# Optimization experiments

Hardware: AMD Instinct MI355X
Metric: run time of the kernel (lower is better)

The kernel has to match this reference:

```python
import jax, jax.numpy as jnp
import numpy as np

B, T, IN, H, OUT = 128, 512, 64, 1024, 1


def _glorot(key, shape, fan_in):
    # mimic nn.Linear default init scale (uniform +-1/sqrt(fan_in))
    bound = 1.0 / np.sqrt(fan_in)
    return jax.random.uniform(key, shape, jnp.float32, -bound, bound)


def setup_inputs() -> dict:
    key = jax.random.key(0)
    ks = jax.random.split(key, 20)
    inp = {
        "x": jax.random.normal(ks[0], (B, T, IN), jnp.float32),
        "boundary": jax.random.normal(ks[1], (B, 2), jnp.float32),
        # layer 0: stacked gate weights, order [i, f, o, g]
        "Wx0": _glorot(ks[2], (4 * H, IN), IN),
        "bx0": _glorot(ks[3], (4 * H,), IN),
        "Uh0": _glorot(ks[4], (4 * H, H), H),
        "bh0": _glorot(ks[5], (4 * H,), H),
        "Wb0": _glorot(ks[6], (H, 2), 2),
        "bb0": _glorot(ks[7], (H,), 2),
        # layer 1
        "Wx1": _glorot(ks[8], (4 * H, H), H),
        "bx1": _glorot(ks[9], (4 * H,), H),
        "Uh1": _glorot(ks[10], (4 * H, H), H),
        "bh1": _glorot(ks[11], (4 * H,), H),
        "Wb1": _glorot(ks[12], (H, 2), 2),
        "bb1": _glorot(ks[13], (H, 2)[:1], 2),
        # output head
        "fcW": _glorot(ks[14], (OUT, H), H),
        "fcb": _glorot(ks[15], (OUT,), H),
    }
    return inp


def _cell(gates, f_extra, c_prev):
    # gates: [B, 4H] pre-activations in order i,f,o,g
    i, f, o, g = jnp.split(gates, 4, axis=-1)
    i = jax.nn.sigmoid(i)
    f = jax.nn.sigmoid(f + f_extra)
    o = jax.nn.sigmoid(o)
    g = jnp.tanh(g)
    c = f * c_prev + i * g
    h = o * jnp.tanh(c)
    return h, c


def reference(x, boundary, Wx0, bx0, Uh0, bh0, Wb0, bb0,
              Wx1, bx1, Uh1, bh1, Wb1, bb1, fcW, fcb):
    batch = x.shape[0]
    Hdim = fcW.shape[1]
    # precompute input projections for layer 0 over all timesteps: [T,B,4H]
    xp0 = jnp.einsum('bti,gi->tbg', x, Wx0) + bx0
    # boundary influence on forget gate, constant over time: [B,H]
    bi0 = boundary @ Wb0.T + bb0
    bi1 = boundary @ Wb1.T + bb1

    zeros = jnp.zeros((batch, Hdim), x.dtype)
    carry0 = (zeros, zeros, zeros, zeros)  # h0, c0, h1, c1

    def step(carry, xp_t):
        h0, c0, h1, c1 = carry
        g0 = xp_t + h0 @ Uh0.T + bh0
        h0n, c0n = _cell(g0, bi0, c0)
        g1 = h0n @ Wx1.T + bx1 + h1 @ Uh1.T + bh1
        h1n, c1n = _cell(g1, bi1, c1)
        return (h0n, c0n, h1n, c1n), None

    (h0, c0, h1, c1), _ = jax.lax.scan(step, carry0, xp0)
    # fc applied to last timestep's top-layer hidden state
    return h1 @ fcW.T + fcb
```

## Files before the change

kernel.cpp:

```cpp
#include <hip/hip_runtime.h>
#include <math.h>


#define Hd 1024
#define Bd 128
#define Td 512
#define INd 64
#define NWG 256
#define NTHR 512

typedef _Float16 f16;
typedef _Float16 half8 __attribute__((ext_vector_type(8)));
typedef float f32x4 __attribute__((ext_vector_type(4)));


__device__ __forceinline__ float fsigm(float x) {
    return __fdividef(1.f, 1.f + __expf(-x));
}
__device__ __forceinline__ float ftanh_(float x) {
    return 1.f - __fdividef(2.f, 1.f + __expf(2.f * x));
}

__global__ __launch_bounds__(512) void init_state(
    const float* __restrict__ bnd, const float* __restrict__ Wb0,
    const float* __restrict__ bb0, const float* __restrict__ Wb1,
    const float* __restrict__ bb1,
    float* __restrict__ bi0, float* __restrict__ bi1,
    f16* __restrict__ h0buf, f16* __restrict__ h1buf,
    unsigned int* __restrict__ sync)
{
    int idx = blockIdx.x * 512 + threadIdx.x;
    int b = idx >> 10;
    int h = idx & 1023;
    float b0v = bnd[b * 2 + 0], b1v = bnd[b * 2 + 1];
    bi0[idx] = b0v * Wb0[h * 2 + 0] + b1v * Wb0[h * 2 + 1] + bb0[h];
    bi1[idx] = b0v * Wb1[h * 2 + 0] + b1v * Wb1[h * 2 + 1] + bb1[h];
    h0buf[idx] = (f16)0.f;  h0buf[idx + Bd * Hd] = (f16)0.f;
    h1buf[idx] = (f16)0.f;  h1buf[idx + Bd * Hd] = (f16)0.f;
    if (idx < 640) sync[idx] = 0u;
}

__global__ __launch_bounds__(512) void xpose(
    const float* __restrict__ x, f16* __restrict__ xT)
{
    int idx = blockIdx.x * 512 + threadIdx.x;
    int b = idx >> 15;
    int t = (idx >> 6) & 511;
    int i = idx & 63;
    xT[((size_t)t * Bd + b) * INd + i] = (f16)x[idx];
}

__global__ __launch_bounds__(NTHR, 2) void lstm_persist(
    const f16* __restrict__ xT,
    f16* __restrict__ h0buf, f16* __restrict__ h1buf,
    const float* __restrict__ bi0, const float* __restrict__ bi1,
    const float* __restrict__ Wx0, const float* __restrict__ bx0,
    const float* __restrict__ Uh0, const float* __restrict__ bh0,
    const float* __restrict__ Wx1, const float* __restrict__ bx1,
    const float* __restrict__ Uh1, const float* __restrict__ bh1,
    const float* __restrict__ fcW, const float* __restrict__ fcb,
    float* __restrict__ out, unsigned int* __restrict__ sync)
{
    const int tid  = threadIdx.x;
    const int w    = tid >> 6;
    const int lane = tid & 63;
    const int n    = lane & 15;
    const int q    = lane >> 4;
    const int wg   = blockIdx.x;
    const int c0wg = wg * 4;
    const int hcol = c0wg + (n & 3);
    const int gid  = n >> 2;
    const bool lowhalf = (w < 4);
    const int p    = lowhalf ? w : (w - 4);
    const int mt   = lowhalf ? 2 * p : 2 * p + 1;
    const size_t S = (size_t)Bd * Hd;

    __shared__ f16 B0[16 * 1096];
    __shared__ float xchg[3072];

    const bool glead = ((wg & 31) == 0);
    unsigned int* garr = sync + 32 + 32 * (wg >> 5);
    int  xcd  = 0;
    bool lead = false;
    unsigned int* relp = nullptr;
    if (tid == 0) {
        asm volatile("s_getreg_b32 %0, hwreg(HW_REG_XCC_ID)" : "=s"(xcd));
        xcd &= 7;
        unsigned r = __hip_atomic_fetch_add(&sync[608 + xcd], 1u,
                         __ATOMIC_RELAXED, __HIP_MEMORY_SCOPE_AGENT);
        lead = (r == 0u);
        relp = sync + 288 + 32 * xcd;
    }

    {
        int nr = tid >> 5;
        int gr = (nr >> 2) * Hd + c0wg + (nr & 3);
        for (int k = tid & 31; k < 1088; k += 32) {
            float v = (k < Hd) ? Uh0[(size_t)gr * Hd + k]
                               : Wx0[(size_t)gr * INd + (k - Hd)];
            B0[nr * 1096 + k] = (f16)v;
        }
    }

    half8 b1f[32];
    {
        const float* Wsrc = lowhalf ? Wx1 : Uh1;
        int gr = gid * Hd + c0wg + (n & 3);
        const float* rp = Wsrc + (size_t)gr * Hd + q * 8;
        #pragma unroll
        for (int kk = 0; kk < 32; ++kk) {
            half8 hv;
            #pragma unroll
            for (int j = 0; j < 8; ++j) hv[j] = (f16)rp[kk * 32 + j];
            b1f[kk] = hv;
        }
    }

    float gb0[4], gb1[4], bia0[4], bia1[4];
    #pragma unroll
    for (int g = 0; g < 4; ++g) {
        gb0[g] = bx0[g * Hd + hcol] + bh0[g * Hd + hcol];
        gb1[g] = bx1[g * Hd + hcol] + bh1[g * Hd + hcol];
    }
    #pragma unroll
    for (int r = 0; r < 4; ++r) {
        int row = mt * 16 + q * 4 + r;
        bia0[r] = bi0[row * Hd + hcol];
        bia1[r] = bi1[row * Hd + hcol];
    }
    f32x4 c0v = {0.f, 0.f, 0.f, 0.f};
    f32x4 c1v = {0.f, 0.f, 0.f, 0.f};

    __syncthreads();

    unsigned epoch = 0;

    for (int s = -1; s <= 511; ++s) {
        const bool do_l0 = (s < 511);
        const bool do_l1 = (s >= 0);
        const int pr = s & 1;
        const f16* h0r = h0buf + (size_t)pr * S;
        f16*       h0w = h0buf + (size_t)(1 - pr) * S;
        const f16* h1r = h1buf + (size_t)(1 - pr) * S;
        f16*       h1w = h1buf + (size_t)pr * S;

        f32x4 a0a = {0.f,0.f,0.f,0.f}, a0b = {0.f,0.f,0.f,0.f};
        f32x4 a1a = {0.f,0.f,0.f,0.f}, a1b = {0.f,0.f,0.f,0.f};

        if (lowhalf) {
            const half8* pA0 = (const half8*)(h0r + (size_t)(2*p*16 + n) * Hd + q*8);
            const half8* pA1 = (const half8*)(h0r + (size_t)((2*p+1)*16 + n) * Hd + q*8);
            const half8* pB  = (const half8*)(&B0[n * 1096 + q * 8]);
            if (do_l0 && do_l1) {
                #pragma unroll
                for (int kk = 0; kk < 32; ++kk) {
                    half8 A0 = pA0[kk*4], A1 = pA1[kk*4], Bl = pB[kk*4];
                    a0a = __builtin_amdgcn_mfma_f32_16x16x32_f16(A0, Bl, a0a, 0,0,0);
                    a0b = __builtin_amdgcn_mfma_f32_16x16x32_f16(A1, Bl, a0b, 0,0,0);
                    a1a = __builtin_amdgcn_mfma_f32_16x16x32_f16(A0, b1f[kk], a1a, 0,0,0);
                    a1b = __builtin_amdgcn_mfma_f32_16x16x32_f16(A1, b1f[kk], a1b, 0,0,0);
                }
            } else if (do_l0) {
                #pragma unroll
                for (int kk = 0; kk < 32; ++kk) {
                    half8 A0 = pA0[kk*4], A1 = pA1[kk*4], Bl = pB[kk*4];
                    a0a = __builtin_amdgcn_mfma_f32_16x16x32_f16(A0, Bl, a0a, 0,0,0);
                    a0b = __builtin_amdgcn_mfma_f32_16x16x32_f16(A1, Bl, a0b, 0,0,0);
                }
            } else {
                #pragma unroll
                for (int kk = 0; kk < 32; ++kk) {
                    half8 A0 = pA0[kk*4], A1 = pA1[kk*4];
                    a1a = __builtin_amdgcn_mfma_f32_16x16x32_f16(A0, b1f[kk], a1a, 0,0,0);
                    a1b = __builtin_amdgcn_mfma_f32_16x16x32_f16(A1, b1f[kk], a1b, 0,0,0);
                }
            }
            if (do_l0) {
                const f16* xt = xT + (size_t)(s + 1) * Bd * INd;
                const half8* pX0 = (const half8*)(xt + (size_t)(2*p*16 + n) * INd + q*8);
                const half8* pX1 = (const half8*)(xt + (size_t)((2*p+1)*16 + n) * INd + q*8);
                #pragma unroll
                for (int kk = 0; kk < 2; ++kk) {
                    half8 Bl = pB[(32 + kk) * 4];
                    a0a = __builtin_amdgcn_mfma_f32_16x16x32_f16(pX0[kk*4], Bl, a0a, 0,0,0);
                    a0b = __builtin_amdgcn_mfma_f32_16x16x32_f16(pX1[kk*4], Bl, a0b, 0,0,0);
                }
            }
        } else if (do_l1) {
            const half8* pH1a = (const half8*)(h1r + (size_t)(2*p*16 + n) * Hd + q*8);
            const half8* pH1b = (const half8*)(h1r + (size_t)((2*p+1)*16 + n) * Hd + q*8);
            #pragma unroll
            for (int kk = 0; kk < 32; ++kk) {
                half8 A0 = pH1a[kk*4], A1 = pH1b[kk*4];
                a1a = __builtin_amdgcn_mfma_f32_16x16x32_f16(A0, b1f[kk], a1a, 0,0,0);
                a1b = __builtin_amdgcn_mfma_f32_16x16x32_f16(A1, b1f[kk], a1b, 0,0,0);
            }
        }

        float* slotA = xchg;
        float* slotB = xchg + 1024;
        float* slotC = xchg + 2048;
        if (lowhalf) {
            if (do_l0) *(f32x4*)&slotA[p * 256 + lane * 4] = a0b;
            if (do_l1) *(f32x4*)&slotB[p * 256 + lane * 4] = a1b;
        } else {
            if (do_l1) *(f32x4*)&slotC[p * 256 + lane * 4] = a1a;
        }
        __syncthreads();

        f32x4 g0acc, g1acc;
        if (lowhalf) {
            g0acc = a0a;
            if (do_l1) g1acc = a1a + *(const f32x4*)&slotC[p * 256 + lane * 4];
        } else {
            if (do_l0) g0acc = *(const f32x4*)&slotA[p * 256 + lane * 4];
            if (do_l1) g1acc = a1b + *(const f32x4*)&slotB[p * 256 + lane * 4];
        }

        auto cell = [&](f32x4 acc, const float* gb, const float* bia,
                        f32x4& cst, f16* hw) {
            #pragma unroll
            for (int r = 0; r < 4; ++r) {
                float own = acc[r];
                float v4  = __shfl_xor(own, 4);
                float v8  = __shfl_xor(own, 8);
                float v12 = __shfl_xor(own, 12);
                float ip = gid==0?own: gid==1?v4 : gid==2?v8 : v12;
                float fp = gid==0?v4 : gid==1?own: gid==2?v12: v8;
                float op = gid==0?v8 : gid==1?v12: gid==2?own: v4;
                float gp = gid==0?v12: gid==1?v8 : gid==2?v4 : own;
                float I = fsigm(ip + gb[0]);
                float F = fsigm(fp + gb[1] + bia[r]);
                float O = fsigm(op + gb[2]);
                float G = ftanh_(gp + gb[3]);
                float c = F * cst[r] + I * G;
                cst[r] = c;
                float h = O * ftanh_(c);
                if (n < 4) {
                    union { f16 hf; unsigned short us; } cv; cv.hf = (f16)h;
                    __hip_atomic_store(
                        (unsigned short*)&hw[(size_t)(mt * 16 + q * 4 + r) * Hd + c0wg + n],
                        cv.us, __ATOMIC_RELAXED, __HIP_MEMORY_SCOPE_AGENT);
                }
            }
        };
        if (do_l0) cell(g0acc, gb0, bia0, c0v, h0w);
        if (do_l1) cell(g1acc, gb1, bia1, c1v, h1w);

        __syncthreads();
        if (tid == 0) {
            const unsigned tgt = epoch + 1u;
            __hip_atomic_fetch_add(garr, 1u, __ATOMIC_RELAXED,
                                   __HIP_MEMORY_SCOPE_AGENT);
            if (glead) {
                while (__hip_atomic_load(garr, __ATOMIC_RELAXED,
                                         __HIP_MEMORY_SCOPE_AGENT) < 32u * tgt)
                    __builtin_amdgcn_s_sleep(1);
                __hip_atomic_fetch_add(sync, 32u, __ATOMIC_RELAXED,
                                       __HIP_MEMORY_SCOPE_AGENT);
            }
            if (lead) {
                while (__hip_atomic_load(sync, __ATOMIC_RELAXED,
                                         __HIP_MEMORY_SCOPE_AGENT) < NWG * tgt)
                    __builtin_amdgcn_s_sleep(1);
                asm volatile("buffer_inv sc1\n\ts_waitcnt vmcnt(0)" ::: "memory");
                __hip_atomic_store(relp, tgt, __ATOMIC_RELAXED,
                                   __HIP_MEMORY_SCOPE_AGENT);
            } else {
                while (__hip_atomic_load(relp, __ATOMIC_RELAXED,
                                         __HIP_MEMORY_SCOPE_AGENT) < tgt)
                    __builtin_amdgcn_s_sleep(1);
                asm volatile("buffer_inv\n\ts_waitcnt vmcnt(0)" ::: "memory");
            }
        }
        epoch++;
        __syncthreads();
    }

    if (blockIdx.x < Bd) {
        int b = blockIdx.x;
        const f16* hf = h1buf + S + (size_t)b * Hd;
        int k = tid * 2;
        float sum = (float)hf[k] * fcW[k] + (float)hf[k + 1] * fcW[k + 1];
        #pragma unroll
        for (int off = 32; off > 0; off >>= 1) sum += __shfl_down(sum, off);
        float* red = xchg;
        if (lane == 0) red[w] = sum;
        __syncthreads();
        if (tid == 0) {
            float t = 0.f;
            #pragma unroll
            for (int i = 0; i < 8; ++i) t += red[i];
            out[b] = t + fcb[0];
        }
    }
}

extern "C" void kernel_launch(void* const* d_in, const int* in_sizes, int n_in,
                              void* d_out, int out_size, void* d_ws, size_t ws_size,
                              hipStream_t stream) {
    const float* x        = (const float*)d_in[0];
    const float* boundary = (const float*)d_in[1];
    const float* Wx0      = (const float*)d_in[2];
    const float* bx0      = (const float*)d_in[3];
    const float* Uh0      = (const float*)d_in[4];
    const float* bh0      = (const float*)d_in[5];
    const float* Wb0      = (const float*)d_in[6];
    const float* bb0      = (const float*)d_in[7];
    const float* Wx1      = (const float*)d_in[8];
    const float* bx1      = (const float*)d_in[9];
    const float* Uh1      = (const float*)d_in[10];
    const float* bh1      = (const float*)d_in[11];
    const float* Wb1      = (const float*)d_in[12];
    const float* bb1      = (const float*)d_in[13];
    const float* fcW      = (const float*)d_in[14];
    const float* fcb      = (const float*)d_in[15];
    float* out = (float*)d_out;

    char* ws = (char*)d_ws;
    f16*   xT    = (f16*)(ws);
    f16*   h0buf = (f16*)(ws + 8388608);
    f16*   h1buf = (f16*)(ws + 8912896);
    float* bi0   = (float*)(ws + 9437184);
    float* bi1   = (float*)(ws + 9961472);
    unsigned int* sync = (unsigned int*)(ws + 10485760);

    init_state<<<256, 512, 0, stream>>>(boundary, Wb0, bb0, Wb1, bb1,
                                        bi0, bi1, h0buf, h1buf, sync);
    xpose<<<8192, 512, 0, stream>>>(x, xT);

    void* args[] = {
        (void*)&xT, (void*)&h0buf, (void*)&h1buf, (void*)&bi0, (void*)&bi1,
        (void*)&Wx0, (void*)&bx0, (void*)&Uh0, (void*)&bh0,
        (void*)&Wx1, (void*)&bx1, (void*)&Uh1, (void*)&bh1,
        (void*)&fcW, (void*)&fcb, (void*)&out, (void*)&sync
    };
    hipLaunchCooperativeKernel((void*)lstm_persist, dim3(NWG), dim3(NTHR),
                               args, 0, stream);
}
```

Baseline: 11.00 ms.

## Retile persistent LSTM to 8 hidden columns by 64 batch rows per workgroup

Workgroups now split work as pairs: each covers 8 hidden columns (all four gates, laid out as two 16-wide N tiles) and half the batch, rather than 4 columns across the full batch. Each wave loads one A fragment per k step and reuses it across two B tiles. Layer 0 is handled entirely by the low waves and layer 1 by the high waves, which cuts the LDS exchange to a single layer-1 partial sum and replaces the three-way gate shuffle with one xor-8 shuffle. The cost is twice the LDS for layer-0 weights and two register-resident layer-1 weight fragments per lane, which raises register pressure under the 2-waves launch bound and may cause spills.

```diff
diff --git a/kernel.cpp b/kernel.cpp
--- a/kernel.cpp
+++ b/kernel.cpp
@@ -67,16 +67,17 @@
     const int n    = lane & 15;
     const int q    = lane >> 4;
     const int wg   = blockIdx.x;
-    const int c0wg = wg * 4;
-    const int hcol = c0wg + (n & 3);
-    const int gid  = n >> 2;
+    const int gb   = wg >> 1;
+    const int bh   = wg & 1;
+    const int hc0  = gb * 8;
+    const int hcol = hc0 + (n & 7);
     const bool lowhalf = (w < 4);
     const int p    = lowhalf ? w : (w - 4);
-    const int mt   = lowhalf ? 2 * p : 2 * p + 1;
+    const int bt   = bh * 64 + p * 16;
     const size_t S = (size_t)Bd * Hd;
 
-    __shared__ f16 B0[16 * 1096];
-    __shared__ float xchg[3072];
+    __shared__ f16 B0[32 * 1096];
+    __shared__ float xchg[2048];
 
     const bool glead = ((wg & 31) == 0);
     unsigned int* garr = sync + 32 + 32 * (wg >> 5);
@@ -93,26 +94,33 @@
     }
 
     {
-        int nr = tid >> 5;
-        int gr = (nr >> 2) * Hd + c0wg + (nr & 3);
-        for (int k = tid & 31; k < 1088; k += 32) {
+        int nr = tid >> 4;
+        int t  = nr >> 4, np = nr & 15;
+        int gr = (t * 2 + (np >> 3)) * Hd + hc0 + (np & 7);
+        for (int k = tid & 15; k < 1088; k += 16) {
             float v = (k < Hd) ? Uh0[(size_t)gr * Hd + k]
                                : Wx0[(size_t)gr * INd + (k - Hd)];
             B0[nr * 1096 + k] = (f16)v;
         }
     }
 
-    half8 b1f[32];
+    half8 b1f0[32], b1f1[32];
     {
         const float* Wsrc = lowhalf ? Wx1 : Uh1;
-        int gr = gid * Hd + c0wg + (n & 3);
-        const float* rp = Wsrc + (size_t)gr * Hd + q * 8;
+        int gr0 = (0 + (n >> 3)) * Hd + hcol;
+        int gr1 = (2 + (n >> 3)) * Hd + hcol;
+        const float* rp0 = Wsrc + (size_t)gr0 * Hd + q * 8;
+        const float* rp1 = Wsrc + (size_t)gr1 * Hd + q * 8;
         #pragma unroll
         for (int kk = 0; kk < 32; ++kk) {
-            half8 hv;
+            half8 h0v, h1v;
             #pragma unroll
-            for (int j = 0; j < 8; ++j) hv[j] = (f16)rp[kk * 32 + j];
-            b1f[kk] = hv;
+            for (int j = 0; j < 8; ++j) {
+                h0v[j] = (f16)rp0[kk * 32 + j];
+                h1v[j] = (f16)rp1[kk * 32 + j];
+            }
+            b1f0[kk] = h0v;
+            b1f1[kk] = h1v;
         }
     }
 
@@ -124,9 +132,9 @@
     }
     #pragma unroll
     for (int r = 0; r < 4; ++r) {
-        int row = mt * 16 + q * 4 + r;
-        bia0[r] = bi0[row * Hd + hcol];
-        bia1[r] = bi1[row * Hd + hcol];
+        int row = bt + q * 4 + r;
+        bia0[r] = bi0[(size_t)row * Hd + hcol];
+        bia1[r] = bi1[(size_t)row * Hd + hcol];
     }
     f32x4 c0v = {0.f, 0.f, 0.f, 0.f};
     f32x4 c1v = {0.f, 0.f, 0.f, 0.f};
@@ -148,104 +156,89 @@
         f32x4 a1a = {0.f,0.f,0.f,0.f}, a1b = {0.f,0.f,0.f,0.f};
 
         if (lowhalf) {
-            const half8* pA0 = (const half8*)(h0r + (size_t)(2*p*16 + n) * Hd + q*8);
-            const half8* pA1 = (const half8*)(h0r + (size_t)((2*p+1)*16 + n) * Hd + q*8);
-            const half8* pB  = (const half8*)(&B0[n * 1096 + q * 8]);
+            const half8* pA  = (const half8*)(h0r + (size_t)(bt + n) * Hd + q*8);
+            const half8* pB0t = (const half8*)(&B0[n        * 1096 + q * 8]);
+            const half8* pB1t = (const half8*)(&B0[(16 + n) * 1096 + q * 8]);
             if (do_l0 && do_l1) {
                 #pragma unroll
                 for (int kk = 0; kk < 32; ++kk) {
-                    half8 A0 = pA0[kk*4], A1 = pA1[kk*4], Bl = pB[kk*4];
-                    a0a = __builtin_amdgcn_mfma_f32_16x16x32_f16(A0, Bl, a0a, 0,0,0);
-                    a0b = __builtin_amdgcn_mfma_f32_16x16x32_f16(A1, Bl, a0b, 0,0,0);
-                    a1a = __builtin_amdgcn_mfma_f32_16x16x32_f16(A0, b1f[kk], a1a, 0,0,0);
-                    a1b = __builtin_amdgcn_mfma_f32_16x16x32_f16(A1, b1f[kk], a1b, 0,0,0);
+                    half8 A = pA[kk*4];
+                    a0a = __builtin_amdgcn_mfma_f32_16x16x32_f16(A, pB0t[kk*4], a0a, 0,0,0);
+                    a0b = __builtin_amdgcn_mfma_f32_16x16x32_f16(A, pB1t[kk*4], a0b, 0,0,0);
+                    a1a = __builtin_amdgcn_mfma_f32_16x16x32_f16(A, b1f0[kk], a1a, 0,0,0);
+                    a1b = __builtin_amdgcn_mfma_f32_16x16x32_f16(A, b1f1[kk], a1b, 0,0,0);
                 }
             } else if (do_l0) {
                 #pragma unroll
                 for (int kk = 0; kk < 32; ++kk) {
-                    half8 A0 = pA0[kk*4], A1 = pA1[kk*4], Bl = pB[kk*4];
-                    a0a = __builtin_amdgcn_mfma_f32_16x16x32_f16(A0, Bl, a0a, 0,0,0);
-                    a0b = __builtin_amdgcn_mfma_f32_16x16x32_f16(A1, Bl, a0b, 0,0,0);
+                    half8 A = pA[kk*4];
+                    a0a = __builtin_amdgcn_mfma_f32_16x16x32_f16(A, pB0t[kk*4], a0a, 0,0,0);
+                    a0b = __builtin_amdgcn_mfma_f32_16x16x32_f16(A, pB1t[kk*4], a0b, 0,0,0);
                 }
             } else {
                 #pragma unroll
                 for (int kk = 0; kk < 32; ++kk) {
-                    half8 A0 = pA0[kk*4], A1 = pA1[kk*4];
-                    a1a = __builtin_amdgcn_mfma_f32_16x16x32_f16(A0, b1f[kk], a1a, 0,0,0);
-                    a1b = __builtin_amdgcn_mfma_f32_16x16x32_f16(A1, b1f[kk], a1b, 0,0,0);
+                    half8 A = pA[kk*4];
+                    a1a = __builtin_amdgcn_mfma_f32_16x16x32_f16(A, b1f0[kk], a1a, 0,0,0);
+                    a1b = __builtin_amdgcn_mfma_f32_16x16x32_f16(A, b1f1[kk], a1b, 0,0,0);
                 }
             }
             if (do_l0) {
                 const f16* xt = xT + (size_t)(s + 1) * Bd * INd;
-                const half8* pX0 = (const half8*)(xt + (size_t)(2*p*16 + n) * INd + q*8);
-                const half8* pX1 = (const half8*)(xt + (size_t)((2*p+1)*16 + n) * INd + q*8);
+                const half8* pX = (const half8*)(xt + (size_t)(bt + n) * INd + q*8);
                 #pragma unroll
                 for (int kk = 0; kk < 2; ++kk) {
-                    half8 Bl = pB[(32 + kk) * 4];
-                    a0a = __builtin_amdgcn_mfma_f32_16x16x32_f16(pX0[kk*4], Bl, a0a, 0,0,0);
-                    a0b = __builtin_amdgcn_mfma_f32_16x16x32_f16(pX1[kk*4], Bl, a0b, 0,0,0);
+                    half8 X = pX[kk*4];
+                    a0a = __builtin_amdgcn_mfma_f32_16x16x32_f16(X, pB0t[(32+kk)*4], a0a, 0,0,0);
+                    a0b = __builtin_amdgcn_mfma_f32_16x16x32_f16(X, pB1t[(32+kk)*4], a0b, 0,0,0);
                 }
             }
         } else if (do_l1) {
-            const half8* pH1a = (const half8*)(h1r + (size_t)(2*p*16 + n) * Hd + q*8);
-            const half8* pH1b = (const half8*)(h1r + (size_t)((2*p+1)*16 + n) * Hd + q*8);
+            const half8* pH = (const half8*)(h1r + (size_t)(bt + n) * Hd + q*8);
             #pragma unroll
             for (int kk = 0; kk < 32; ++kk) {
-                half8 A0 = pH1a[kk*4], A1 = pH1b[kk*4];
-                a1a = __builtin_amdgcn_mfma_f32_16x16x32_f16(A0, b1f[kk], a1a, 0,0,0);
-                a1b = __builtin_amdgcn_mfma_f32_16x16x32_f16(A1, b1f[kk], a1b, 0,0,0);
-            }
-        }
-
-        float* slotA = xchg;
-        float* slotB = xchg + 1024;
-        float* slotC = xchg + 2048;
-        if (lowhalf) {
-            if (do_l0) *(f32x4*)&slotA[p * 256 + lane * 4] = a0b;
-            if (do_l1) *(f32x4*)&slotB[p * 256 + lane * 4] = a1b;
-        } else {
-            if (do_l1) *(f32x4*)&slotC[p * 256 + lane * 4] = a1a;
+                half8 A = pH[kk*4];
+                a1a = __builtin_amdgcn_mfma_f32_16x16x32_f16(A, b1f0[kk], a1a, 0,0,0);
+                a1b = __builtin_amdgcn_mfma_f32_16x16x32_f16(A, b1f1[kk], a1b, 0,0,0);
+            }
+        }
+
+        if (lowhalf && do_l1) {
+            *(f32x4*)&xchg[p * 512 +       lane * 4] = a1a;
+            *(f32x4*)&xchg[p * 512 + 256 + lane * 4] = a1b;
         }
         __syncthreads();
-
-        f32x4 g0acc, g1acc;
-        if (lowhalf) {
-            g0acc = a0a;
-            if (do_l1) g1acc = a1a + *(const f32x4*)&slotC[p * 256 + lane * 4];
-        } else {
-            if (do_l0) g0acc = *(const f32x4*)&slotA[p * 256 + lane * 4];
-            if (do_l1) g1acc = a1b + *(const f32x4*)&slotB[p * 256 + lane * 4];
-        }
-
-        auto cell = [&](f32x4 acc, const float* gb, const float* bia,
-                        f32x4& cst, f16* hw) {
+        f32x4 g1a, g1b;
+        if (!lowhalf && do_l1) {
+            g1a = a1a + *(const f32x4*)&xchg[p * 512 +       lane * 4];
+            g1b = a1b + *(const f32x4*)&xchg[p * 512 + 256 + lane * 4];
+        }
+
+        auto cell = [&](f32x4 accA, f32x4 accB, const float* gbx,
+                        const float* bia, f32x4& cst, f16* hw) {
             #pragma unroll
             for (int r = 0; r < 4; ++r) {
-                float own = acc[r];
-                float v4  = __shfl_xor(own, 4);
-                float v8  = __shfl_xor(own, 8);
-                float v12 = __shfl_xor(own, 12);
-                float ip = gid==0?own: gid==1?v4 : gid==2?v8 : v12;
-                float fp = gid==0?v4 : gid==1?own: gid==2?v12: v8;
-                float op = gid==0?v8 : gid==1?v12: gid==2?own: v4;
-                float gp = gid==0?v12: gid==1?v8 : gid==2?v4 : own;
-                float I = fsigm(ip + gb[0]);
-                float F = fsigm(fp + gb[1] + bia[r]);
-                float O = fsigm(op + gb[2]);
-                float G = ftanh_(gp + gb[3]);
+                float t0  = accA[r];
+                float t1  = accB[r];
+                float t0x = __shfl_xor(t0, 8);
+                float t1x = __shfl_xor(t1, 8);
+                float I = fsigm(t0  + gbx[0]);
+                float F = fsigm(t0x + gbx[1] + bia[r]);
+                float O = fsigm(t1  + gbx[2]);
+                float G = ftanh_(t1x + gbx[3]);
                 float c = F * cst[r] + I * G;
                 cst[r] = c;
                 float h = O * ftanh_(c);
-                if (n < 4) {
+                if (n < 8) {
                     union { f16 hf; unsigned short us; } cv; cv.hf = (f16)h;
                     __hip_atomic_store(
-                        (unsigned short*)&hw[(size_t)(mt * 16 + q * 4 + r) * Hd + c0wg + n],
+                        (unsigned short*)&hw[(size_t)(bt + q * 4 + r) * Hd + hc0 + n],
                         cv.us, __ATOMIC_RELAXED, __HIP_MEMORY_SCOPE_AGENT);
                 }
             }
         };
-        if (do_l0) cell(g0acc, gb0, bia0, c0v, h0w);
-        if (do_l1) cell(g1acc, gb1, bia1, c1v, h1w);
+        if (lowhalf) { if (do_l0) cell(a0a, a0b, gb0, bia0, c0v, h0w); }
+        else         { if (do_l1) cell(g1a, g1b, gb1, bia1, c1v, h1w); }
 
         __syncthreads();
         if (tid == 0) {
```

New measurement: 10.75 ms. 1.02x faster.

## Double workgroup to 16 waves, each wave owns one row tile, weights in LDS

Applied to the files above, without the earlier changes.

Workgroups grow from 8 to 16 waves. Each wave now handles a single 16-row batch tile instead of two, so the per-step MFMA chain per wave is roughly halved. The Wx1/Uh1 weight fragments move from per-wave registers into a larger shared buffer (48 rows), along with Uh0/Wx0. Layer-0 and layer-1 cells are split across the two wave halves, and only the layer-1 partial sums are exchanged through LDS. The costs are more LDS traffic (weights are reread every step), a roughly 105 KB LDS footprint, and a launch-bounds hint of 4 that is optimistic for 1024-thread blocks.

```diff
diff --git a/kernel.cpp b/kernel.cpp
--- a/kernel.cpp
+++ b/kernel.cpp
@@ -7,7 +7,7 @@
 #define Td 512
 #define INd 64
 #define NWG 256
-#define NTHR 512
+#define NTHR 1024
 
 typedef _Float16 f16;
 typedef _Float16 half8 __attribute__((ext_vector_type(8)));
@@ -50,7 +50,7 @@
     xT[((size_t)t * Bd + b) * INd + i] = (f16)x[idx];
 }
 
-__global__ __launch_bounds__(NTHR, 2) void lstm_persist(
+__global__ __launch_bounds__(NTHR, 4) void lstm_persist(
     const f16* __restrict__ xT,
     f16* __restrict__ h0buf, f16* __restrict__ h1buf,
     const float* __restrict__ bi0, const float* __restrict__ bi1,
@@ -70,13 +70,12 @@
     const int c0wg = wg * 4;
     const int hcol = c0wg + (n & 3);
     const int gid  = n >> 2;
-    const bool lowhalf = (w < 4);
-    const int p    = lowhalf ? w : (w - 4);
-    const int mt   = lowhalf ? 2 * p : 2 * p + 1;
+    const bool lowhalf = (w < 8);
+    const int p    = lowhalf ? w : (w - 8);
     const size_t S = (size_t)Bd * Hd;
 
-    __shared__ f16 B0[16 * 1096];
-    __shared__ float xchg[3072];
+    __shared__ f16 WL[48 * 1096];
+    __shared__ float xchg[2048];
 
     const bool glead = ((wg & 31) == 0);
     unsigned int* garr = sync + 32 + 32 * (wg >> 5);
@@ -93,43 +92,37 @@
     }
 
     {
-        int nr = tid >> 5;
-        int gr = (nr >> 2) * Hd + c0wg + (nr & 3);
-        for (int k = tid & 31; k < 1088; k += 32) {
-            float v = (k < Hd) ? Uh0[(size_t)gr * Hd + k]
-                               : Wx0[(size_t)gr * INd + (k - Hd)];
-            B0[nr * 1096 + k] = (f16)v;
-        }
-    }
-
-    half8 b1f[32];
+        int nr = tid >> 4;
+        if (nr < 48) {
+            int loc = nr & 15;
+            int gr = (loc >> 2) * Hd + c0wg + (loc & 3);
+            if (nr < 16) {
+                for (int k = tid & 15; k < 1088; k += 16) {
+                    float v = (k < Hd) ? Uh0[(size_t)gr * Hd + k]
+                                       : Wx0[(size_t)gr * INd + (k - Hd)];
+                    WL[nr * 1096 + k] = (f16)v;
+                }
+            } else {
+                const float* Wsrc = (nr < 32) ? Wx1 : Uh1;
+                for (int k = tid & 15; k < 1024; k += 16)
+                    WL[nr * 1096 + k] = (f16)Wsrc[(size_t)gr * Hd + k];
+            }
+        }
+    }
+
+    float gbx[4], bia[4];
     {
-        const float* Wsrc = lowhalf ? Wx1 : Uh1;
-        int gr = gid * Hd + c0wg + (n & 3);
-        const float* rp = Wsrc + (size_t)gr * Hd + q * 8;
+        const float* bxp = lowhalf ? bx0 : bx1;
+        const float* bhp = lowhalf ? bh0 : bh1;
+        const float* bip = lowhalf ? bi0 : bi1;
         #pragma unroll
-        for (int kk = 0; kk < 32; ++kk) {
-            half8 hv;
-            #pragma unroll
-            for (int j = 0; j < 8; ++j) hv[j] = (f16)rp[kk * 32 + j];
-            b1f[kk] = hv;
-        }
-    }
-
-    float gb0[4], gb1[4], bia0[4], bia1[4];
-    #pragma unroll
-    for (int g = 0; g < 4; ++g) {
-        gb0[g] = bx0[g * Hd + hcol] + bh0[g * Hd + hcol];
-        gb1[g] = bx1[g * Hd + hcol] + bh1[g * Hd + hcol];
-    }
-    #pragma unroll
-    for (int r = 0; r < 4; ++r) {
-        int row = mt * 16 + q * 4 + r;
-        bia0[r] = bi0[row * Hd + hcol];
-        bia1[r] = bi1[row * Hd + hcol];
-    }
-    f32x4 c0v = {0.f, 0.f, 0.f, 0.f};
-    f32x4 c1v = {0.f, 0.f, 0.f, 0.f};
+        for (int g = 0; g < 4; ++g)
+            gbx[g] = bxp[g * Hd + hcol] + bhp[g * Hd + hcol];
+        #pragma unroll
+        for (int r = 0; r < 4; ++r)
+            bia[r] = bip[(size_t)(p * 16 + q * 4 + r) * Hd + hcol];
+    }
+    f32x4 cst = {0.f, 0.f, 0.f, 0.f};
 
     __syncthreads();
 
@@ -144,81 +137,59 @@
         const f16* h1r = h1buf + (size_t)(1 - pr) * S;
         f16*       h1w = h1buf + (size_t)pr * S;
 
-        f32x4 a0a = {0.f,0.f,0.f,0.f}, a0b = {0.f,0.f,0.f,0.f};
-        f32x4 a1a = {0.f,0.f,0.f,0.f}, a1b = {0.f,0.f,0.f,0.f};
+        f32x4 a0 = {0.f,0.f,0.f,0.f};
+        f32x4 a1 = {0.f,0.f,0.f,0.f};
 
         if (lowhalf) {
-            const half8* pA0 = (const half8*)(h0r + (size_t)(2*p*16 + n) * Hd + q*8);
-            const half8* pA1 = (const half8*)(h0r + (size_t)((2*p+1)*16 + n) * Hd + q*8);
-            const half8* pB  = (const half8*)(&B0[n * 1096 + q * 8]);
+            const half8* pA  = (const half8*)(h0r + (size_t)(p*16 + n) * Hd + q*8);
+            const half8* pB0 = (const half8*)(&WL[n         * 1096 + q * 8]);
+            const half8* pB1 = (const half8*)(&WL[(16 + n)  * 1096 + q * 8]);
             if (do_l0 && do_l1) {
-                #pragma unroll
+                #pragma unroll 8
                 for (int kk = 0; kk < 32; ++kk) {
-                    half8 A0 = pA0[kk*4], A1 = pA1[kk*4], Bl = pB[kk*4];
-                    a0a = __builtin_amdgcn_mfma_f32_16x16x32_f16(A0, Bl, a0a, 0,0,0);
-                    a0b = __builtin_amdgcn_mfma_f32_16x16x32_f16(A1, Bl, a0b, 0,0,0);
-                    a1a = __builtin_amdgcn_mfma_f32_16x16x32_f16(A0, b1f[kk], a1a, 0,0,0);
-                    a1b = __builtin_amdgcn_mfma_f32_16x16x32_f16(A1, b1f[kk], a1b, 0,0,0);
+                    half8 A = pA[kk*4];
+                    a0 = __builtin_amdgcn_mfma_f32_16x16x32_f16(A, pB0[kk*4], a0, 0,0,0);
+                    a1 = __builtin_amdgcn_mfma_f32_16x16x32_f16(A, pB1[kk*4], a1, 0,0,0);
                 }
             } else if (do_l0) {
-                #pragma unroll
+                #pragma unroll 8
                 for (int kk = 0; kk < 32; ++kk) {
-                    half8 A0 = pA0[kk*4], A1 = pA1[kk*4], Bl = pB[kk*4];
-                    a0a = __builtin_amdgcn_mfma_f32_16x16x32_f16(A0, Bl, a0a, 0,0,0);
-                    a0b = __builtin_amdgcn_mfma_f32_16x16x32_f16(A1, Bl, a0b, 0,0,0);
+                    half8 A = pA[kk*4];
+                    a0 = __builtin_amdgcn_mfma_f32_16x16x32_f16(A, pB0[kk*4], a0, 0,0,0);
                 }
             } else {
-                #pragma unroll
+                #pragma unroll 8
                 for (int kk = 0; kk < 32; ++kk) {
-                    half8 A0 = pA0[kk*4], A1 = pA1[kk*4];
-                    a1a = __builtin_amdgcn_mfma_f32_16x16x32_f16(A0, b1f[kk], a1a, 0,0,0);
-                    a1b = __builtin_amdgcn_mfma_f32_16x16x32_f16(A1, b1f[kk], a1b, 0,0,0);
+                    half8 A = pA[kk*4];
+                    a1 = __builtin_amdgcn_mfma_f32_16x16x32_f16(A, pB1[kk*4], a1, 0,0,0);
                 }
             }
             if (do_l0) {
                 const f16* xt = xT + (size_t)(s + 1) * Bd * INd;
-                const half8* pX0 = (const half8*)(xt + (size_t)(2*p*16 + n) * INd + q*8);
-                const half8* pX1 = (const half8*)(xt + (size_t)((2*p+1)*16 + n) * INd + q*8);
+                const half8* pX = (const half8*)(xt + (size_t)(p*16 + n) * INd + q*8);
                 #pragma unroll
-                for (int kk = 0; kk < 2; ++kk) {
-                    half8 Bl = pB[(32 + kk) * 4];
-                    a0a = __builtin_amdgcn_mfma_f32_16x16x32_f16(pX0[kk*4], Bl, a0a, 0,0,0);
-                    a0b = __builtin_amdgcn_mfma_f32_16x16x32_f16(pX1[kk*4], Bl, a0b, 0,0,0);
-                }
+                for (int kk = 0; kk < 2; ++kk)
+                    a0 = __builtin_amdgcn_mfma_f32_16x16x32_f16(
+                             pX[kk*4], pB0[(32 + kk) * 4], a0, 0,0,0);
             }
         } else if (do_l1) {
-            const half8* pH1a = (const half8*)(h1r + (size_t)(2*p*16 + n) * Hd + q*8);
-            const half8* pH1b = (const half8*)(h1r + (size_t)((2*p+1)*16 + n) * Hd + q*8);
-            #pragma unroll
+            const half8* pA  = (const half8*)(h1r + (size_t)(p*16 + n) * Hd + q*8);
+            const half8* pB1 = (const half8*)(&WL[(32 + n) * 1096 + q * 8]);
+            #pragma unroll 8
             for (int kk = 0; kk < 32; ++kk) {
-                half8 A0 = pH1a[kk*4], A1 = pH1b[kk*4];
-                a1a = __builtin_amdgcn_mfma_f32_16x16x32_f16(A0, b1f[kk], a1a, 0,0,0);
-                a1b = __builtin_amdgcn_mfma_f32_16x16x32_f16(A1, b1f[kk], a1b, 0,0,0);
-            }
-        }
-
-        float* slotA = xchg;
-        float* slotB = xchg + 1024;
-        float* slotC = xchg + 2048;
-        if (lowhalf) {
-            if (do_l0) *(f32x4*)&slotA[p * 256 + lane * 4] = a0b;
-            if (do_l1) *(f32x4*)&slotB[p * 256 + lane * 4] = a1b;
-        } else {
-            if (do_l1) *(f32x4*)&slotC[p * 256 + lane * 4] = a1a;
-        }
+                half8 A = pA[kk*4];
+                a1 = __builtin_amdgcn_mfma_f32_16x16x32_f16(A, pB1[kk*4], a1, 0,0,0);
+            }
+        }
+
+        if (lowhalf && do_l1)
+            *(f32x4*)&xchg[p * 256 + lane * 4] = a1;
         __syncthreads();
-
-        f32x4 g0acc, g1acc;
-        if (lowhalf) {
-            g0acc = a0a;
-            if (do_l1) g1acc = a1a + *(const f32x4*)&slotC[p * 256 + lane * 4];
-        } else {
-            if (do_l0) g0acc = *(const f32x4*)&slotA[p * 256 + lane * 4];
-            if (do_l1) g1acc = a1b + *(const f32x4*)&slotB[p * 256 + lane * 4];
-        }
-
-        auto cell = [&](f32x4 acc, const float* gb, const float* bia,
-                        f32x4& cst, f16* hw) {
+        f32x4 g1;
+        if (!lowhalf && do_l1)
+            g1 = a1 + *(const f32x4*)&xchg[p * 256 + lane * 4];
+
+        auto cell = [&](f32x4 acc, f16* hw) {
             #pragma unroll
             for (int r = 0; r < 4; ++r) {
                 float own = acc[r];
@@ -229,23 +200,23 @@
                 float fp = gid==0?v4 : gid==1?own: gid==2?v12: v8;
                 float op = gid==0?v8 : gid==1?v12: gid==2?own: v4;
                 float gp = gid==0?v12: gid==1?v8 : gid==2?v4 : own;
-                float I = fsigm(ip + gb[0]);
-                float F = fsigm(fp + gb[1] + bia[r]);
-                float O = fsigm(op + gb[2]);
-                float G = ftanh_(gp + gb[3]);
+                float I = fsigm(ip + gbx[0]);
+                float F = fsigm(fp + gbx[1] + bia[r]);
+                float O = fsigm(op + gbx[2]);
+                float G = ftanh_(gp + gbx[3]);
                 float c = F * cst[r] + I * G;
                 cst[r] = c;
                 float h = O * ftanh_(c);
                 if (n < 4) {
                     union { f16 hf; unsigned short us; } cv; cv.hf = (f16)h;
                     __hip_atomic_store(
-                        (unsigned short*)&hw[(size_t)(mt * 16 + q * 4 + r) * Hd + c0wg + n],
+                        (unsigned short*)&hw[(size_t)(p * 16 + q * 4 + r) * Hd + c0wg + n],
                         cv.us, __ATOMIC_RELAXED, __HIP_MEMORY_SCOPE_AGENT);
                 }
             }
         };
-        if (do_l0) cell(g0acc, gb0, bia0, c0v, h0w);
-        if (do_l1) cell(g1acc, gb1, bia1, c1v, h1w);
+        if (lowhalf) { if (do_l0) cell(a0, h0w); }
+        else         { if (do_l1) cell(g1, h1w); }
 
         __syncthreads();
         if (tid == 0) {
@@ -279,18 +250,19 @@
 
     if (blockIdx.x < Bd) {
         int b = blockIdx.x;
-        const f16* hf = h1buf + S + (size_t)b * Hd;
-        int k = tid * 2;
-        float sum = (float)hf[k] * fcW[k] + (float)hf[k + 1] * fcW[k + 1];
-        #pragma unroll
-        for (int off = 32; off > 0; off >>= 1) sum += __shfl_down(sum, off);
-        float* red = xchg;
-        if (lane == 0) red[w] = sum;
+        if (tid < 512) {
+            const f16* hf = h1buf + S + (size_t)b * Hd;
+            int k = tid * 2;
+            float sum = (float)hf[k] * fcW[k] + (float)hf[k + 1] * fcW[k + 1];
+            #pragma unroll
+            for (int off = 32; off > 0; off >>= 1) sum += __shfl_down(sum, off);
+            if (lane == 0) xchg[w] = sum;
+        }
         __syncthreads();
         if (tid == 0) {
             float t = 0.f;
             #pragma unroll
-            for (int i = 0; i < 8; ++i) t += red[i];
+            for (int i = 0; i < 8; ++i) t += xchg[i];
             out[b] = t + fcb[0];
         }
     }
```

After: 10.42 ms. -5.3%, faster.
